# Optimization experiments

Measured on AMD Instinct MI355X. Metric: run time of the kernel, lower is better.

## Reference

```python
import jax, jax.numpy as jnp
import numpy as np

H = 256   # hidden_size
B = 64    # batch_size
LP = 2048 # passage length
LQ = 64   # question length


def _linear(x, W, b):
    # torch nn.Linear: y = x @ W.T + b
    return jnp.matmul(x, W.T) + b


def _gru_cell(x, h, w_ih, w_hh, b_ih, b_hh):
    # torch GRUCell semantics: x is input, h is hidden state
    gi = jnp.matmul(x, w_ih.T) + b_ih   # [B, 3*2H]
    gh = jnp.matmul(h, w_hh.T) + b_hh
    i_r, i_z, i_n = jnp.split(gi, 3, axis=-1)
    h_r, h_z, h_n = jnp.split(gh, 3, axis=-1)
    r = jax.nn.sigmoid(i_r + h_r)
    z = jax.nn.sigmoid(i_z + h_z)
    n = jnp.tanh(i_n + r * h_n)
    return (1.0 - z) * n + z * h


def setup_inputs() -> dict:
    key = jax.random.key(0)
    ks = jax.random.split(key, 17)
    s = lambda i, shape: jax.random.normal(ks[i], shape, dtype=jnp.float32) * 0.05
    return {
        "passEnc": jax.random.normal(ks[0], (LP, B, 2 * H), dtype=jnp.float32),
        "quesEnc": jax.random.normal(ks[1], (LQ, B, 2 * H), dtype=jnp.float32),
        "WQu_W": s(2, (H, 2 * H)), "WQu_b": s(3, (H,)),
        "WQv_W": s(4, (H, H)),     "WQv_b": s(5, (H,)),
        "WPh_W": s(6, (H, 2 * H)), "WPh_b": s(7, (H,)),
        "Wah_W": s(8, (H, 2 * H)), "Wah_b": s(9, (H,)),
        "Vt1": s(10, (B, H, 1)),
        "Vt2": s(11, (B, H, 1)),
        "VQr": s(12, (1, 1, H)),
        "gru_wih": s(13, (6 * H, 2 * H)), "gru_whh": s(14, (6 * H, 2 * H)),
        "gru_bih": s(15, (6 * H,)),       "gru_bhh": s(16, (6 * H,)),
    }


def reference(passEnc, quesEnc, WQu_W, WQu_b, WQv_W, WQv_b, WPh_W, WPh_b,
              Wah_W, Wah_b, Vt1, Vt2, VQr, gru_wih, gru_whh, gru_bih, gru_bhh):
    # --- question-aware initial state rQ ---
    # temp: [lQ, B, H] (VQr path broadcasts over lQ and B)
    temp = jnp.tanh(_linear(quesEnc, WQu_W, WQu_b) + _linear(VQr, WQv_W, WQv_b))
    sQ = jnp.einsum('qbh,bh->bq', temp, Vt1[..., 0])          # [B, lQ]
    a = jax.nn.softmax(sQ, axis=1)
    rQ = jnp.einsum('bq,qbd->bd', a, quesEnc)                 # [B, 2H]

    passP = _linear(passEnc, WPh_W, WPh_b)                    # [lP, B, H], reused both steps

    def pointer_step(rQ):
        temp2 = jnp.tanh(passP + _linear(rQ, Wah_W, Wah_b))   # [lP, B, H]
        sP = jnp.einsum('pbh,bh->bp', temp2, Vt2[..., 0])     # [B, lP]
        aP = jax.nn.softmax(sP, axis=1)
        ct = jnp.einsum('bp,pbd->bd', aP, passEnc)            # [B, 2H]
        return aP, ct

    aP1, ct = pointer_step(rQ)
    rQ = _gru_cell(rQ, ct, gru_wih, gru_whh, gru_bih, gru_bhh)
    aP2, _ = pointer_step(rQ)
    return (aP1, aP2)


if __name__ == "__main__":
    out = reference(**setup_inputs())
    print(out[0].shape, out[1].shape)
```

## Files before the change

kernel.cpp:

```cpp
#include <hip/hip_runtime.h>
#include <math.h>


constexpr int Bn   = 64;
constexpr int Hn   = 256;
constexpr int D2H  = 512;
constexpr int LPn  = 2048;
constexpr int LQn  = 64;

typedef __attribute__((ext_vector_type(8))) short bf16x8;
typedef __attribute__((ext_vector_type(4))) float f32x4;

typedef const __attribute__((address_space(1))) unsigned int* gup;
typedef __attribute__((address_space(3))) unsigned int* lup;
__device__ inline void async16(const void* g, void* l) {
  __builtin_amdgcn_global_load_lds((gup)g, (lup)l, 16, 0, 0);
}

__device__ inline float waveAllSum(float v) {
  #pragma unroll
  for (int o = 32; o > 0; o >>= 1) v += __shfl_xor(v, o, 64);
  return v;
}
__device__ inline float waveAllMax(float v) {
  #pragma unroll
  for (int o = 32; o > 0; o >>= 1) v = fmaxf(v, __shfl_xor(v, o, 64));
  return v;
}

__device__ inline short f2bf_rtne(float f) {
  union { float f; unsigned u; } v; v.f = f;
  unsigned r = v.u + 0x7FFF + ((v.u >> 16) & 1);
  return (short)(r >> 16);
}
__device__ inline unsigned pk2(float lo, float hi) {
  union { float f; unsigned u; } a, b; a.f = lo; b.f = hi;
  return __builtin_amdgcn_perm(b.u + 0x8000u, a.u + 0x8000u, 0x07060302u);
}
__device__ inline bf16x8 cvt8(f32x4 a0, f32x4 a1) {
  union { unsigned u[4]; bf16x8 v; } r;
  r.u[0] = pk2(a0[0], a0[1]);
  r.u[1] = pk2(a0[2], a0[3]);
  r.u[2] = pk2(a1[0], a1[1]);
  r.u[3] = pk2(a1[2], a1[3]);
  return r.v;
}

__global__ __launch_bounds__(256) void k_wcvt(const float* __restrict__ WQu,
                                              const float* __restrict__ WPh,
                                              short* __restrict__ q16,
                                              short* __restrict__ p16) {
  int e = (blockIdx.x * 256 + threadIdx.x) * 4;
  const float* src; short* dst; int off;
  if (e < 131072) { src = WQu; dst = q16; off = e; }
  else            { src = WPh; dst = p16; off = e - 131072; }
  f32x4 f = *(const f32x4*)&src[off];
  short4 h;
  h.x = f2bf_rtne(f[0]); h.y = f2bf_rtne(f[1]);
  h.z = f2bf_rtne(f[2]); h.w = f2bf_rtne(f[3]);
  *(short4*)&dst[off] = h;
}

__global__ __launch_bounds__(256) void k_v2(const float* __restrict__ VQr,
                                            const float* __restrict__ WQv_W,
                                            const float* __restrict__ WQv_b,
                                            float* __restrict__ v2) {
  __shared__ float s[256];
  int t = threadIdx.x;
  s[t] = VQr[t];
  __syncthreads();
  float acc = WQv_b[t];
  for (int k = 0; k < 256; ++k) acc += s[k] * WQv_W[t * 256 + k];
  v2[t] = acc;
}

__global__ __launch_bounds__(256, 3) void k_mfma(
    const float* __restrict__ A,
    const short* __restrict__ Wb,
    const float* __restrict__ bias,
    const float* __restrict__ u,
    const float* __restrict__ vt,
    short* __restrict__ pp,
    float* __restrict__ sOut,
    int ustride, int sstride)
{
  __shared__ union {
    struct { float As[32 * 256]; short Bs[16 * 512]; } m;
    float sred[256];
  } sm;
  const int t = threadIdx.x;
  const int w = t >> 6, l = t & 63, l15 = l & 15, quad = l >> 4;
  const int wm = w >> 1, wn = w & 1;
  const int lin   = blockIdx.x;
  const int grp   = lin >> 4;
  const int half  = (lin & 15) >> 3;
  const int mtile = grp * 8 + (lin & 7);
  const long bm = (long)mtile * 128;
  const int n0 = half * 128;

  f32x4 acc[4][4];
  #pragma unroll
  for (int i = 0; i < 4; ++i)
    #pragma unroll
    for (int j = 0; j < 4; ++j)
      acc[i][j] = (f32x4)0.f;

  const int fcA = ((t >> 7) << 3) | (((t >> 4) & 3) << 1) | ((t >> 6) & 1);
  const float* gA = A + (bm + (t & 15)) * 512 + fcA * 4;
  const int cB = (((t >> 6) & 1) << 2) | ((t >> 4) & 3);
  const short* gB = Wb + (size_t)(n0 + ((t >> 7) << 4) + (t & 15)) * 512 + cB * 8;
  char* lA = (char*)sm.m.As + t * 16;
  char* lB = (char*)sm.m.Bs + t * 16;

  for (int k0 = 0; k0 < 512; k0 += 64) {
    #pragma unroll
    for (int it = 0; it < 8; ++it)
      async16(gA + it * 8192 + k0, lA + it * 4096);
    #pragma unroll
    for (int it = 0; it < 4; ++it)
      async16(gB + it * 16384 + k0, lB + it * 4096);
    __syncthreads();
    const int lb = l * 4;
    #pragma unroll
    for (int ks = 0; ks < 2; ++ks) {
      bf16x8 af[4], bfv[4];
      #pragma unroll
      for (int i = 0; i < 4; ++i) {
        const int pl = ((wm * 4 + i) * 4 + ks * 2) * 256;
        f32x4 p0 = *(const f32x4*)&sm.m.As[pl + lb];
        f32x4 p1 = *(const f32x4*)&sm.m.As[pl + 256 + lb];
        af[i] = cvt8(p0, p1);
      }
      #pragma unroll
      for (int j = 0; j < 4; ++j) {
        const int rg = ((wn * 4 + j) * 2 + ks) * 512;
        bfv[j] = *(const bf16x8*)&sm.m.Bs[rg + l * 8];
      }
      #pragma unroll
      for (int i = 0; i < 4; ++i)
        #pragma unroll
        for (int j = 0; j < 4; ++j)
          acc[i][j] = __builtin_amdgcn_mfma_f32_16x16x32_bf16(af[i], bfv[j], acc[i][j], 0, 0, 0);
    }
    __syncthreads();
  }

  short* ppt = pp ? pp + (((size_t)mtile * 2 + half) * 16384 + (size_t)w * 4096 + l * 8)
                  : nullptr;
  float srow[4][4];
  #pragma unroll
  for (int i = 0; i < 4; ++i) {
    #pragma unroll
    for (int r = 0; r < 4; ++r) srow[i][r] = 0.f;
    unsigned pk[8];
    const int bb = i * 16 + quad * 4;
    #pragma unroll
    for (int j = 0; j < 4; ++j) {
      const int n = n0 + wn * 64 + j * 16 + l15;
      const float bn = bias[n];
      float v0 = acc[i][j][0] + bn, v1 = acc[i][j][1] + bn;
      float v2 = acc[i][j][2] + bn, v3 = acc[i][j][3] + bn;
      if (ppt) { pk[j * 2] = pk2(v0, v1); pk[j * 2 + 1] = pk2(v2, v3); }
      srow[i][0] += tanhf(v0 + u[ustride * (bb + 0) + n]) * vt[(bb + 0) * 256 + n];
      srow[i][1] += tanhf(v1 + u[ustride * (bb + 1) + n]) * vt[(bb + 1) * 256 + n];
      srow[i][2] += tanhf(v2 + u[ustride * (bb + 2) + n]) * vt[(bb + 2) * 256 + n];
      srow[i][3] += tanhf(v3 + u[ustride * (bb + 3) + n]) * vt[(bb + 3) * 256 + n];
    }
    if (ppt) {
      uint4 s0 = {pk[0], pk[1], pk[2], pk[3]};
      uint4 s1 = {pk[4], pk[5], pk[6], pk[7]};
      *(uint4*)&ppt[i * 1024]       = s0;
      *(uint4*)&ppt[i * 1024 + 512] = s1;
    }
  }
  #pragma unroll
  for (int off = 1; off < 16; off <<= 1)
    #pragma unroll
    for (int i = 0; i < 4; ++i)
      #pragma unroll
      for (int r = 0; r < 4; ++r)
        srow[i][r] += __shfl_xor(srow[i][r], off, 64);
  if (l15 == 0)
    #pragma unroll
    for (int i = 0; i < 4; ++i)
      #pragma unroll
      for (int r = 0; r < 4; ++r)
        sm.sred[wn * 128 + wm * 64 + i * 16 + quad * 4 + r] = srow[i][r];
  __syncthreads();
  if (t < 128) {
    float s = sm.sred[t] + sm.sred[128 + t];
    int b = t & 63;
    int pg = mtile * 2 + (t >> 6);
    atomicAdd(&sOut[(size_t)b * sstride + pg], s);
  }
}

__global__ __launch_bounds__(256) void k_sp2(const short* __restrict__ pp,
                                             const float* __restrict__ u2,
                                             const float* __restrict__ vt,
                                             float* __restrict__ sP) {
  __shared__ float sred[256];
  const int g = blockIdx.x, t = threadIdx.x;
  const int w = t >> 6, l = t & 63, l15 = l & 15, quad = l >> 4;
  const int wm = w >> 1, wn = w & 1;
  const int n0 = (g & 1) * 128;
  const short* src = pp + (size_t)g * 16384 + (size_t)w * 4096 + l * 8;
  float srow[4][4];
  #pragma unroll
  for (int i = 0; i < 4; ++i) {
    uint4 q0 = *(const uint4*)&src[i * 1024];
    uint4 q1 = *(const uint4*)&src[i * 1024 + 512];
    unsigned pk[8] = {q0.x, q0.y, q0.z, q0.w, q1.x, q1.y, q1.z, q1.w};
    #pragma unroll
    for (int r = 0; r < 4; ++r) srow[i][r] = 0.f;
    const int bb = i * 16 + quad * 4;
    #pragma unroll
    for (int j = 0; j < 4; ++j) {
      const int n = n0 + wn * 64 + j * 16 + l15;
      #pragma unroll
      for (int r = 0; r < 4; ++r) {
        unsigned word = pk[j * 2 + (r >> 1)];
        unsigned bits = (r & 1) ? (word & 0xFFFF0000u) : (word << 16);
        float val = __uint_as_float(bits);
        srow[i][r] += tanhf(val + u2[(bb + r) * 256 + n]) * vt[(bb + r) * 256 + n];
      }
    }
  }
  #pragma unroll
  for (int off = 1; off < 16; off <<= 1)
    #pragma unroll
    for (int i = 0; i < 4; ++i)
      #pragma unroll
      for (int r = 0; r < 4; ++r)
        srow[i][r] += __shfl_xor(srow[i][r], off, 64);
  if (l15 == 0)
    #pragma unroll
    for (int i = 0; i < 4; ++i)
      #pragma unroll
      for (int r = 0; r < 4; ++r)
        sred[wn * 128 + wm * 64 + i * 16 + quad * 4 + r] = srow[i][r];
  __syncthreads();
  if (t < 128) {
    float s = sred[t] + sred[128 + t];
    int b = t & 63;
    int pg = (g >> 1) * 2 + (t >> 6);
    atomicAdd(&sP[(size_t)b * LPn + pg], s);
  }
}

__global__ __launch_bounds__(256) void k_rq_u1(const float* __restrict__ sQ,
                                               const float* __restrict__ quesEnc,
                                               const float* __restrict__ Wah,
                                               const float* __restrict__ Wah_b,
                                               float* __restrict__ rQ,
                                               float* __restrict__ u1) {
  int b = blockIdx.x, tid = threadIdx.x;
  __shared__ float s_a[LQn];
  __shared__ float s_r[D2H];
  if (tid < 64) {
    float s = sQ[b * LQn + tid];
    float m = waveAllMax(s);
    float e = expf(s - m);
    float sum = waveAllSum(e);
    s_a[tid] = e / sum;
  }
  __syncthreads();
  #pragma unroll
  for (int rep = 0; rep < 2; ++rep) {
    int d = tid + rep * 256;
    float acc = 0.f;
    for (int q = 0; q < LQn; ++q)
      acc += s_a[q] * quesEnc[(size_t)(q * Bn + b) * D2H + d];
    s_r[d] = acc;
    rQ[b * D2H + d] = acc;
  }
  __syncthreads();
  float accu = Wah_b[tid];
  const float* wr = Wah + (size_t)tid * 512;
  for (int k4 = 0; k4 < 128; ++k4) {
    f32x4 wv = *(const f32x4*)&wr[k4 * 4];
    f32x4 rv = *(const f32x4*)&s_r[k4 * 4];
    accu += wv[0] * rv[0] + wv[1] * rv[1] + wv[2] * rv[2] + wv[3] * rv[3];
  }
  u1[b * Hn + tid] = accu;
}

__global__ __launch_bounds__(256) void k_softmax(const float* __restrict__ sP,
                                                 float* __restrict__ out) {
  int b = blockIdx.x, tid = threadIdx.x;
  int lane = tid & 63, wid = tid >> 6;
  __shared__ float red[4];
  float v[8];
  float m = -1e30f;
  #pragma unroll
  for (int i = 0; i < 8; ++i) {
    v[i] = sP[b * LPn + i * 256 + tid];
    m = fmaxf(m, v[i]);
  }
  m = waveAllMax(m);
  if (lane == 0) red[wid] = m;
  __syncthreads();
  m = fmaxf(fmaxf(red[0], red[1]), fmaxf(red[2], red[3]));
  float s = 0.f;
  #pragma unroll
  for (int i = 0; i < 8; ++i) { v[i] = expf(v[i] - m); s += v[i]; }
  s = waveAllSum(s);
  __syncthreads();
  if (lane == 0) red[wid] = s;
  __syncthreads();
  s = red[0] + red[1] + red[2] + red[3];
  float inv = 1.0f / s;
  #pragma unroll
  for (int i = 0; i < 8; ++i) out[b * LPn + i * 256 + tid] = v[i] * inv;
}

__global__ __launch_bounds__(256) void k_ct(const float* __restrict__ aP,
                                            const float* __restrict__ passEnc,
                                            float* __restrict__ ct) {
  int b = blockIdx.x, pc = blockIdx.y, tid = threadIdx.x;
  int dg = tid & 127;
  int pg = tid >> 7;
  f32x4 acc = (f32x4)0.f;
  #pragma unroll
  for (int pp = 0; pp < 32; ++pp) {
    int p = pc * 64 + pg * 32 + pp;
    float a = aP[b * LPn + p];
    acc += a * *(const f32x4*)&passEnc[((size_t)p * Bn + b) * D2H + dg * 4];
  }
  __shared__ f32x4 sacc[256];
  sacc[tid] = acc;
  __syncthreads();
  if (pg == 0) {
    acc += sacc[tid + 128];
    float* dst = &ct[b * D2H + dg * 4];
    atomicAdd(dst + 0, acc[0]);
    atomicAdd(dst + 1, acc[1]);
    atomicAdd(dst + 2, acc[2]);
    atomicAdd(dst + 3, acc[3]);
  }
}

__global__ __launch_bounds__(256) void k_gih(const float* __restrict__ rQ,
                                             const float* __restrict__ ct,
                                             const float* __restrict__ wih,
                                             const float* __restrict__ whh,
                                             const float* __restrict__ bih,
                                             const float* __restrict__ bhh,
                                             float* __restrict__ gi,
                                             float* __restrict__ gh) {
  __shared__ float sw[16 * 512];
  int blk = blockIdx.x;
  bool isH = blk >= 96;
  const float* W = isH ? whh : wih;
  const float* X = isH ? ct : rQ;
  const float* bias = isH ? bhh : bih;
  float* G = isH ? gh : gi;
  int r0 = (isH ? blk - 96 : blk) * 16;
  int t = threadIdx.x;
  #pragma unroll
  for (int it = 0; it < 8; ++it) {
    int f4 = it * 256 + t;
    *(f32x4*)&sw[f4 * 4] = *(const f32x4*)&W[(size_t)r0 * 512 + f4 * 4];
  }
  __syncthreads();
  int b = t & 63;
  int rbase = (t >> 6) * 4;
  const float* x = X + b * 512;
  float acc[4];
  #pragma unroll
  for (int oo = 0; oo < 4; ++oo) acc[oo] = bias[r0 + rbase + oo];
  for (int k4 = 0; k4 < 128; ++k4) {
    f32x4 xv = *(const f32x4*)&x[k4 * 4];
    #pragma unroll
    for (int oo = 0; oo < 4; ++oo) {
      f32x4 wv = *(const f32x4*)&sw[(rbase + oo) * 512 + k4 * 4];
      acc[oo] += wv[0] * xv[0] + wv[1] * xv[1] + wv[2] * xv[2] + wv[3] * xv[3];
    }
  }
  #pragma unroll
  for (int oo = 0; oo < 4; ++oo)
    G[b * 1536 + r0 + rbase + oo] = acc[oo];
}

__global__ __launch_bounds__(256) void k_gates(const float* __restrict__ gi,
                                               const float* __restrict__ gh,
                                               const float* __restrict__ ct,
                                               float* __restrict__ rQ2) {
  int idx = blockIdx.x * 256 + threadIdx.x;
  int b = idx >> 9;
  int j = idx & 511;
  const float* gib = gi + b * 1536;
  const float* ghb = gh + b * 1536;
  float r = 1.f / (1.f + expf(-(gib[j] + ghb[j])));
  float z = 1.f / (1.f + expf(-(gib[512 + j] + ghb[512 + j])));
  float n = tanhf(gib[1024 + j] + r * ghb[1024 + j]);
  rQ2[b * D2H + j] = (1.f - z) * n + z * ct[b * D2H + j];
}

__global__ __launch_bounds__(256) void k_u2(const float* __restrict__ rQ2,
                                            const float* __restrict__ Wah,
                                            const float* __restrict__ Wah_b,
                                            float* __restrict__ u2) {
  int m = blockIdx.x, n = threadIdx.x;
  __shared__ float s_r[D2H];
  s_r[n]       = rQ2[m * D2H + n];
  s_r[n + 256] = rQ2[m * D2H + n + 256];
  __syncthreads();
  float acc = Wah_b[n];
  const float* wr = Wah + (size_t)n * 512;
  for (int k4 = 0; k4 < 128; ++k4) {
    f32x4 wv = *(const f32x4*)&wr[k4 * 4];
    f32x4 rv = *(const f32x4*)&s_r[k4 * 4];
    acc += wv[0] * rv[0] + wv[1] * rv[1] + wv[2] * rv[2] + wv[3] * rv[3];
  }
  u2[m * Hn + n] = acc;
}

extern "C" void kernel_launch(void* const* d_in, const int* in_sizes, int n_in,
                              void* d_out, int out_size, void* d_ws, size_t ws_size,
                              hipStream_t stream) {
  const float* passEnc  = (const float*)d_in[0];
  const float* quesEnc  = (const float*)d_in[1];
  const float* WQu_W    = (const float*)d_in[2];
  const float* WQu_b    = (const float*)d_in[3];
  const float* WQv_W    = (const float*)d_in[4];
  const float* WQv_b    = (const float*)d_in[5];
  const float* WPh_W    = (const float*)d_in[6];
  const float* WPh_b    = (const float*)d_in[7];
  const float* Wah_W    = (const float*)d_in[8];
  const float* Wah_b    = (const float*)d_in[9];
  const float* Vt1      = (const float*)d_in[10];
  const float* Vt2      = (const float*)d_in[11];
  const float* VQr      = (const float*)d_in[12];
  const float* gru_wih  = (const float*)d_in[13];
  const float* gru_whh  = (const float*)d_in[14];
  const float* gru_bih  = (const float*)d_in[15];
  const float* gru_bhh  = (const float*)d_in[16];
  float* out = (float*)d_out;

  float* ws = (float*)d_ws;
  float* v2    = ws;
  float* rQ    = v2 + 256;
  float* u1    = rQ + 32768;
  float* u2    = u1 + 16384;
  float* sP    = u2 + 16384;
  float* ct    = sP + 131072;
  float* gi    = ct + 32768;
  float* gh    = gi + 98304;
  float* rQ2   = gh + 98304;
  float* sQ    = rQ2 + 32768;
  short* wqu16 = (short*)(sQ + 4096);
  short* wph16 = wqu16 + 131072;
  short* pp16  = wph16 + 131072;

  hipMemsetAsync(sQ, 0, Bn * LQn * sizeof(float), stream);
  hipMemsetAsync(sP, 0, Bn * LPn * sizeof(float), stream);
  hipMemsetAsync(ct, 0, Bn * D2H * sizeof(float), stream);

  k_wcvt<<<256, 256, 0, stream>>>(WQu_W, WPh_W, wqu16, wph16);
  k_v2<<<1, 256, 0, stream>>>(VQr, WQv_W, WQv_b, v2);

  k_mfma<<<LQn * Bn / 64, 256, 0, stream>>>(
      quesEnc, wqu16, WQu_b, v2, Vt1, nullptr, sQ, 0, LQn);
  k_rq_u1<<<Bn, 256, 0, stream>>>(sQ, quesEnc, Wah_W, Wah_b, rQ, u1);

  k_mfma<<<LPn * Bn / 64, 256, 0, stream>>>(
      passEnc, wph16, WPh_b, u1, Vt2, pp16, sP, Hn, LPn);
  k_softmax<<<Bn, 256, 0, stream>>>(sP, out);

  k_ct<<<dim3(Bn, 32), 256, 0, stream>>>(out, passEnc, ct);

  k_gih<<<192, 256, 0, stream>>>(rQ, ct, gru_wih, gru_whh, gru_bih, gru_bhh, gi, gh);
  k_gates<<<Bn * D2H / 256, 256, 0, stream>>>(gi, gh, ct, rQ2);
  k_u2<<<Bn, 256, 0, stream>>>(rQ2, Wah_W, Wah_b, u2);

  hipMemsetAsync(sP, 0, Bn * LPn * sizeof(float), stream);
  k_sp2<<<LPn * Bn / 64, 256, 0, stream>>>(pp16, u2, Vt2, sP);
  k_softmax<<<Bn, 256, 0, stream>>>(sP, out + Bn * LPn);
}
```

Baseline: 832.3 us.

## Double-buffer GEMM K-loop with async prefetch and XOR-swizzled LDS layout

Changes the MFMA GEMM main loop from single-buffered 64-wide K steps to double-buffered 32-wide K steps. The next stage is issued with async global-to-LDS loads while the current tile is multiplied, so load latency can overlap compute. The LDS layout becomes row-major with an XOR swizzle on the chunk index to avoid bank conflicts on fragment reads. LDS usage stays the same, but the loop now has twice as many iterations and barriers. Overlap is uncertain because the async loads may not have completed by the next barrier without an explicit wait.

```diff
diff --git a/kernel.cpp b/kernel.cpp
--- a/kernel.cpp
+++ b/kernel.cpp
@@ -85,7 +85,7 @@
     int ustride, int sstride)
 {
   __shared__ union {
-    struct { float As[32 * 256]; short Bs[16 * 512]; } m;
+    struct { float As[2][4096]; short Bs[2][4096]; } m;
     float sred[256];
   } sm;
   const int t = threadIdx.x;
@@ -105,45 +105,50 @@
     for (int j = 0; j < 4; ++j)
       acc[i][j] = (f32x4)0.f;
 
-  const int fcA = ((t >> 7) << 3) | (((t >> 4) & 3) << 1) | ((t >> 6) & 1);
-  const float* gA = A + (bm + (t & 15)) * 512 + fcA * 4;
-  const int cB = (((t >> 6) & 1) << 2) | ((t >> 4) & 3);
-  const short* gB = Wb + (size_t)(n0 + ((t >> 7) << 4) + (t & 15)) * 512 + cB * 8;
-  char* lA = (char*)sm.m.As + t * 16;
-  char* lB = (char*)sm.m.Bs + t * 16;
-
-  for (int k0 = 0; k0 < 512; k0 += 64) {
-    #pragma unroll
-    for (int it = 0; it < 8; ++it)
-      async16(gA + it * 8192 + k0, lA + it * 4096);
-    #pragma unroll
-    for (int it = 0; it < 4; ++it)
-      async16(gB + it * 16384 + k0, lB + it * 4096);
+  const float* gA = A + (bm + (t >> 3)) * 512 + (((t & 7) ^ ((t >> 3) & 7)) << 2);
+  const short* gB = Wb + (size_t)(n0 + (t >> 2)) * 512 + (((t & 3) ^ ((t >> 2) & 3)) << 3);
+
+  #define STAGE(buf, k0)                                                     \
+    do {                                                                     \
+      char* lA_ = (char*)&sm.m.As[buf][0] + t * 16;                          \
+      char* lB_ = (char*)&sm.m.Bs[buf][0] + t * 16;                          \
+      _Pragma("unroll")                                                      \
+      for (int it = 0; it < 4; ++it)                                         \
+        async16(gA + it * 16384 + (k0), lA_ + it * 4096);                    \
+      _Pragma("unroll")                                                      \
+      for (int it = 0; it < 2; ++it)                                         \
+        async16(gB + it * 32768 + (k0), lB_ + it * 4096);                    \
+    } while (0)
+
+  STAGE(0, 0);
+  __syncthreads();
+  for (int s = 0; s < 16; ++s) {
+    const int cur = s & 1;
+    if (s < 15) STAGE(cur ^ 1, (s + 1) * 32);
+    const float* As = &sm.m.As[cur][0];
+    const short* Bs = &sm.m.Bs[cur][0];
+    bf16x8 af[4], bfv[4];
+    #pragma unroll
+    for (int i = 0; i < 4; ++i) {
+      const int R = wm * 64 + i * 16 + l15;
+      const float* base = &As[R * 32];
+      f32x4 p0 = *(const f32x4*)(base + (((quad * 2) ^ (l15 & 7)) << 2));
+      f32x4 p1 = *(const f32x4*)(base + (((quad * 2 + 1) ^ (l15 & 7)) << 2));
+      af[i] = cvt8(p0, p1);
+    }
+    #pragma unroll
+    for (int j = 0; j < 4; ++j) {
+      const int R = wn * 64 + j * 16 + l15;
+      bfv[j] = *(const bf16x8*)&Bs[R * 32 + ((quad ^ (l15 & 3)) << 3)];
+    }
+    #pragma unroll
+    for (int i = 0; i < 4; ++i)
+      #pragma unroll
+      for (int j = 0; j < 4; ++j)
+        acc[i][j] = __builtin_amdgcn_mfma_f32_16x16x32_bf16(af[i], bfv[j], acc[i][j], 0, 0, 0);
     __syncthreads();
-    const int lb = l * 4;
-    #pragma unroll
-    for (int ks = 0; ks < 2; ++ks) {
-      bf16x8 af[4], bfv[4];
-      #pragma unroll
-      for (int i = 0; i < 4; ++i) {
-        const int pl = ((wm * 4 + i) * 4 + ks * 2) * 256;
-        f32x4 p0 = *(const f32x4*)&sm.m.As[pl + lb];
-        f32x4 p1 = *(const f32x4*)&sm.m.As[pl + 256 + lb];
-        af[i] = cvt8(p0, p1);
-      }
-      #pragma unroll
-      for (int j = 0; j < 4; ++j) {
-        const int rg = ((wn * 4 + j) * 2 + ks) * 512;
-        bfv[j] = *(const bf16x8*)&sm.m.Bs[rg + l * 8];
-      }
-      #pragma unroll
-      for (int i = 0; i < 4; ++i)
-        #pragma unroll
-        for (int j = 0; j < 4; ++j)
-          acc[i][j] = __builtin_amdgcn_mfma_f32_16x16x32_bf16(af[i], bfv[j], acc[i][j], 0, 0, 0);
-    }
-    __syncthreads();
-  }
+  }
+  #undef STAGE
 
   short* ppt = pp ? pp + (((size_t)mtile * 2 + half) * 16384 + (size_t)w * 4096 + l * 8)
                   : nullptr;
```

Measured after the change: 767.7 us. 7.8% less time.
